# Performance work log

Hardware: AMD Instinct MI355X
Metric: run time of the kernel (lower is better)

Reference implementation:

```python
import jax, jax.numpy as jnp
import numpy as np
from jax import lax

B, N, D_IN = 256, 1024, 3
HID, ACT, HORIZON = 256, 6, 50


def _params(key):
    ks = jax.random.split(key, 24)
    w = lambda k, s: (jax.random.normal(k, s, jnp.float32) * 0.05)
    p = {}
    # PointNet encoder: per-point shared MLP 3->64->128->512, max-pool
    p['enc_w1'], p['enc_b1'] = w(ks[0], (D_IN, 64)), jnp.zeros((64,), jnp.float32)
    p['enc_w2'], p['enc_b2'] = w(ks[1], (64, 128)), jnp.zeros((128,), jnp.float32)
    p['enc_w3'], p['enc_b3'] = w(ks[2], (128, 512)), jnp.zeros((512,), jnp.float32)
    # mlp 512->256->128->hidden
    p['mlp_w1'], p['mlp_b1'] = w(ks[3], (512, 256)), jnp.zeros((256,), jnp.float32)
    p['mlp_w2'], p['mlp_b2'] = w(ks[4], (256, 128)), jnp.zeros((128,), jnp.float32)
    p['mlp_w3'], p['mlp_b3'] = w(ks[5], (128, HID)), jnp.zeros((HID,), jnp.float32)
    # GRU cell (PyTorch layout): W_ih [3H, in], W_hh [3H, H]
    p['W_ih'] = w(ks[6], (3 * HID, ACT))
    p['W_hh'] = w(ks[7], (3 * HID, HID))
    p['b_ih'] = jnp.zeros((3 * HID,), jnp.float32)
    p['b_hh'] = jnp.zeros((3 * HID,), jnp.float32)
    # out_mlp hidden->64->64->6
    p['out_w1'], p['out_b1'] = w(ks[8], (HID, 64)), jnp.zeros((64,), jnp.float32)
    p['out_w2'], p['out_b2'] = w(ks[9], (64, 64)), jnp.zeros((64,), jnp.float32)
    p['out_w3'], p['out_b3'] = w(ks[10], (64, ACT)), jnp.zeros((ACT,), jnp.float32)
    return p


def setup_inputs() -> dict:
    key = jax.random.key(0)
    k_data, k_p = jax.random.split(key)
    inp = {'data': jax.random.normal(k_data, (B, N, D_IN), jnp.float32), 'horizon': HORIZON}
    inp.update(_params(k_p))
    return inp


def reference(data, enc_w1, enc_b1, enc_w2, enc_b2, enc_w3, enc_b3,
              mlp_w1, mlp_b1, mlp_w2, mlp_b2, mlp_w3, mlp_b3,
              W_ih, W_hh, b_ih, b_hh,
              out_w1, out_b1, out_w2, out_b2, out_w3, out_b3,
              horizon):
    # PointNet encoder: shared per-point MLP + max-pool over points -> [B, 512]
    x = jax.nn.relu(data @ enc_w1 + enc_b1)
    x = jax.nn.relu(x @ enc_w2 + enc_b2)
    x = jax.nn.relu(x @ enc_w3 + enc_b3)
    h = jnp.max(x, axis=1)
    # init GRU hidden state
    g = jax.nn.relu(h @ mlp_w1 + mlp_b1)
    g = jax.nn.relu(g @ mlp_w2 + mlp_b2)
    gru_h = g @ mlp_w3 + mlp_b3  # [B, HID]

    def gru_cell(x_t, h_prev):
        gi = x_t @ W_ih.T + b_ih  # [B, 3H]
        gh = h_prev @ W_hh.T + b_hh
        i_r, i_z, i_n = jnp.split(gi, 3, axis=-1)
        h_r, h_z, h_n = jnp.split(gh, 3, axis=-1)
        r = jax.nn.sigmoid(i_r + h_r)
        z = jax.nn.sigmoid(i_z + h_z)
        n = jnp.tanh(i_n + r * h_n)
        return (1.0 - z) * n + z * h_prev

    def out_mlp(hh):
        o = jax.nn.relu(hh @ out_w1 + out_b1)
        o = jax.nn.relu(o @ out_w2 + out_b2)
        return o @ out_w3 + out_b3

    def step(carry, _):
        gi, gh_ = carry
        gh_ = gru_cell(gi, gh_)
        dw = out_mlp(gh_)
        gi = gi + dw
        return (gi, gh_), (dw, gi)

    init_in = jnp.zeros((data.shape[0], ACT), jnp.float32)
    _, (dws, ws) = lax.scan(step, (init_in, gru_h), None, length=int(horizon))
    # scan stacks time-first: [T, B, 6] -> [B, T, 6]
    return jnp.transpose(dws, (1, 0, 2)), jnp.transpose(ws, (1, 0, 2))
```

## Files before the change

### kernel.cpp

```cpp
#include <hip/hip_runtime.h>
#include <math.h>

#define B_    256
#define NPTS  1024
#define T_    50


__global__ __launch_bounds__(256) void prep_kernel(
    const float* __restrict__ whh, float* __restrict__ wp,
    unsigned* __restrict__ henc) {
  int idx = blockIdx.x * 256 + threadIdx.x;
  if (idx < 196608) {
    int c = idx & 3;
    int r = idx >> 2;
    int t2 = r & 255;
    int q = r >> 8;
    int j = q % 3;
    int k4 = q / 3;
    wp[idx] = whh[(j * 256 + t2) * 256 + (k4 * 4 + c)];
  }
  if (idx < 131072) henc[idx] = 0u;
}

__global__ __launch_bounds__(1024) void enc_kernel(
    const float* __restrict__ data,
    const float* __restrict__ w1, const float* __restrict__ b1,
    const float* __restrict__ w2, const float* __restrict__ b2,
    const float* __restrict__ w3, const float* __restrict__ b3,
    unsigned* __restrict__ henc) {
  __shared__ float h2t[2][128][66];
  const int t = threadIdx.x;
  const int b = blockIdx.x >> 1;
  const int half = blockIdx.x & 1;
  const int lane = t & 63;
  const int wv = __builtin_amdgcn_readfirstlane(t >> 6);

  float m[32];
#pragma unroll
  for (int o = 0; o < 32; ++o) m[o] = 0.0f;
  const float* __restrict__ w3b = w3 + wv * 32;

#pragma unroll 1
  for (int pair = 0; pair < 4; ++pair) {
#pragma unroll
    for (int tt = 0; tt < 2; ++tt) {
      const int ptg = b * NPTS + half * 512 + (pair * 2 + tt) * 64 + lane;
      const float x0 = data[ptg * 3], x1 = data[ptg * 3 + 1], x2 = data[ptg * 3 + 2];
      float a[8];
#pragma unroll
      for (int c = 0; c < 8; ++c) a[c] = b2[wv * 8 + c];
#pragma unroll 4
      for (int j = 0; j < 64; ++j) {
        float hj = fmaf(x0, w1[j], fmaf(x1, w1[64 + j], fmaf(x2, w1[128 + j], b1[j])));
        hj = fmaxf(hj, 0.0f);
        const float* __restrict__ w2r = w2 + j * 128 + wv * 8;
#pragma unroll
        for (int c = 0; c < 8; ++c) a[c] = fmaf(hj, w2r[c], a[c]);
      }
#pragma unroll
      for (int c = 0; c < 8; ++c) h2t[tt][wv * 8 + c][lane] = fmaxf(a[c], 0.0f);
    }
    __syncthreads();

    float acc0[32], acc1[32];
#pragma unroll
    for (int o = 0; o < 32; ++o) {
      acc0[o] = b3[wv * 32 + o];
      acc1[o] = acc0[o];
    }
#pragma unroll 4
    for (int k = 0; k < 128; ++k) {
      const float hk0 = h2t[0][k][lane];
      const float hk1 = h2t[1][k][lane];
      const float* __restrict__ wr = w3b + k * 512;
#pragma unroll
      for (int o = 0; o < 32; ++o) {
        const float w = wr[o];
        acc0[o] = fmaf(hk0, w, acc0[o]);
        acc1[o] = fmaf(hk1, w, acc1[o]);
      }
    }
#pragma unroll
    for (int o = 0; o < 32; ++o)
      m[o] = fmaxf(fmaxf(m[o], acc0[o]), acc1[o]);
    __syncthreads();
  }

#pragma unroll
  for (int off = 32; off > 0; off >>= 1) {
#pragma unroll
    for (int o = 0; o < 32; ++o) m[o] = fmaxf(m[o], __shfl_xor(m[o], off, 64));
  }
  if (lane == 0) {
    unsigned* __restrict__ hr = henc + b * 512 + wv * 32;
#pragma unroll
    for (int o = 0; o < 32; ++o) atomicMax(hr + o, __float_as_uint(m[o]));
  }
}

__device__ __forceinline__ double fexp(double x) {
  const double n = rint(x * 1.44269504088896338700e+00);
  const double r = fma(-n, 1.90821492927058770002e-10,
                       fma(-n, 6.93147180369123816490e-01, x));
  double p = 1.0 / 6227020800.0;
  p = fma(p, r, 1.0 / 479001600.0);
  p = fma(p, r, 1.0 / 39916800.0);
  p = fma(p, r, 1.0 / 3628800.0);
  p = fma(p, r, 1.0 / 362880.0);
  p = fma(p, r, 1.0 / 40320.0);
  p = fma(p, r, 1.0 / 5040.0);
  p = fma(p, r, 1.0 / 720.0);
  p = fma(p, r, 1.0 / 120.0);
  p = fma(p, r, 1.0 / 24.0);
  p = fma(p, r, 1.0 / 6.0);
  p = fma(p, r, 0.5);
  p = fma(p, r, 1.0);
  p = fma(p, r, 1.0);
  return ldexp(p, (int)n);
}
__device__ __forceinline__ double fsigm(double x) { return 1.0 / (1.0 + fexp(-x)); }
__device__ __forceinline__ double ftanh(double y) {
  const double e = fexp(-2.0 * y);
  return (1.0 - e) / (1.0 + e);
}

__global__ __launch_bounds__(576) void gru_kernel(
    const float* __restrict__ henc,
    const float* __restrict__ mw1, const float* __restrict__ mb1,
    const float* __restrict__ mw2, const float* __restrict__ mb2,
    const float* __restrict__ mw3, const float* __restrict__ mb3,
    const float* __restrict__ wih, const float* __restrict__ wp,
    const float* __restrict__ bih, const float* __restrict__ bhh,
    const float* __restrict__ ow1, const float* __restrict__ ob1,
    const float* __restrict__ ow2, const float* __restrict__ ob2,
    const float* __restrict__ ow3, const float* __restrict__ ob3,
    float* __restrict__ dout) {
  __shared__ __align__(16) double h_l[256];
  __shared__ double pp[3][256];
  __shared__ __align__(16) float ow1f[16384];
  __shared__ __align__(16) float ow2f[4096];
  __shared__ float ow3f[384];
  __shared__ float wihf[4608];
  __shared__ float bihf[768];
  __shared__ double o1_l[64];
  __shared__ double o2_l[64];
  __shared__ double gia_l[6];

  const int t = threadIdx.x;
  const int s = blockIdx.x;

  for (int i = t; i < 4608; i += 576) wihf[i] = wih[i];
  for (int i = t; i < 768; i += 576) bihf[i] = bih[i];

  double* const g1_l = (double*)ow1f;
  double* const g2_l = (double*)ow1f + 256;

  if (t < 256) {
    const float* __restrict__ hrow = henc + (s << 9);
    double a = (double)mb1[t];
#pragma unroll 4
    for (int k = 0; k < 512; ++k)
      a = fma((double)hrow[k], (double)mw1[k * 256 + t], a);
    g1_l[t] = fmax(a, 0.0);
  }
  __syncthreads();
  if (t < 128) {
    double a = (double)mb2[t];
#pragma unroll 4
    for (int k = 0; k < 256; ++k) a = fma(g1_l[k], (double)mw2[k * 128 + t], a);
    g2_l[t] = fmax(a, 0.0);
  }
  __syncthreads();
  if (t < 256) {
    double a = (double)mb3[t];
#pragma unroll 4
    for (int k = 0; k < 128; ++k) a = fma(g2_l[k], (double)mw3[k * 256 + t], a);
    h_l[t] = a;
  }
  if (t < 6) gia_l[t] = 0.0;
  __syncthreads();

  for (int i = t; i < 16384; i += 576) ow1f[i] = ow1[i];
  for (int i = t; i < 4096; i += 576) ow2f[i] = ow2[i];
  if (t < 384) ow3f[t] = ow3[t];

  const int c = t & 255;
  const int hh = (t >> 8) & 1;
  const int khome = hh << 5;
  const double br = (t < 512 && hh == 0) ? (double)bhh[c] : 0.0;
  const double bz = (t < 512 && hh == 0) ? (double)bhh[256 + c] : 0.0;
  const double bn = (t < 512 && hh == 0) ? (double)bhh[512 + c] : 0.0;
  double hreg = (t < 256) ? h_l[c] : 0.0;
  const float* const wpc = wp + c * 4;

  const int ln = t & 63;
  double ob1d = 0.0, ob2d = 0.0, ob3d = 0.0;
  if (t >= 512) {
    ob1d = (double)ob1[ln];
    ob2d = (double)ob2[ln];
    if (ln < 6) ob3d = (double)ob3[ln];
  }

  double ar, az, an;

#define MV_K(kk) {                                                           \
    const float* p_ = wpc + (khome + (kk)) * 3072;                           \
    const float4 wr = *(const float4*)(p_);                                  \
    const float4 wz = *(const float4*)(p_ + 1024);                           \
    const float4 wn = *(const float4*)(p_ + 2048);                           \
    const double2 ha = *(const double2*)(h_l + ((khome + (kk)) << 2));       \
    const double2 hb = *(const double2*)(h_l + ((khome + (kk)) << 2) + 2);   \
    ar = fma(ha.x, (double)wr.x, ar); ar = fma(ha.y, (double)wr.y, ar);      \
    ar = fma(hb.x, (double)wr.z, ar); ar = fma(hb.y, (double)wr.w, ar);      \
    az = fma(ha.x, (double)wz.x, az); az = fma(ha.y, (double)wz.y, az);      \
    az = fma(hb.x, (double)wz.z, az); az = fma(hb.y, (double)wz.w, az);      \
    an = fma(ha.x, (double)wn.x, an); an = fma(ha.y, (double)wn.y, an);      \
    an = fma(hb.x, (double)wn.z, an); an = fma(hb.y, (double)wn.w, an);      \
  }

  if (t < 512) {
    ar = br; az = bz; an = bn;
#pragma unroll 2
    for (int kk = 0; kk < 32; ++kk) MV_K(kk)
    if (hh) { pp[0][c] = ar; pp[1][c] = az; pp[2][c] = an; }
  }
  __syncthreads();

#pragma unroll 1
  for (int step = 0; step < T_; ++step) {
    if (t < 256) {
      const double cr = ar + pp[0][c];
      const double cz = az + pp[1][c];
      const double cn = an + pp[2][c];
      double gr = (double)bihf[c], gz = (double)bihf[256 + c],
             gn = (double)bihf[512 + c];
#pragma unroll
      for (int a = 0; a < 6; ++a) {
        const double xa = gia_l[a];
        gr = fma((double)wihf[c * 6 + a], xa, gr);
        gz = fma((double)wihf[(256 + c) * 6 + a], xa, gz);
        gn = fma((double)wihf[(512 + c) * 6 + a], xa, gn);
      }
      const double rv = fsigm(cr + gr);
      const double zv = fsigm(cz + gz);
      const double nv = ftanh(fma(rv, cn, gn));
      hreg = fma(zv, hreg - nv, nv);
      h_l[c] = hreg;
    }
    if (t < 512) { ar = br; az = bz; an = bn; }
    __syncthreads();

    if (t < 512) {
#pragma unroll 2
      for (int kk = 0; kk < 32; ++kk) MV_K(kk)
      if (hh) { pp[0][c] = ar; pp[1][c] = az; pp[2][c] = an; }
    } else {
      double a0 = ob1d, a1 = 0.0;
#pragma unroll 4
      for (int k = 0; k < 128; ++k) {
        a0 = fma(h_l[k], (double)ow1f[k * 64 + ln], a0);
        a1 = fma(h_l[128 + k], (double)ow1f[(128 + k) * 64 + ln], a1);
      }
      o1_l[ln] = fmax(a0 + a1, 0.0);
      __builtin_amdgcn_wave_barrier();
      double b0 = ob2d;
#pragma unroll 4
      for (int k = 0; k < 64; ++k)
        b0 = fma(o1_l[k], (double)ow2f[k * 64 + ln], b0);
      o2_l[ln] = fmax(b0, 0.0);
      __builtin_amdgcn_wave_barrier();
      if (ln < 6) {
        double a = ob3d;
#pragma unroll 4
        for (int k = 0; k < 64; ++k)
          a = fma(o2_l[k], (double)ow3f[k * 6 + ln], a);
        const double gi_new = gia_l[ln] + a;
        gia_l[ln] = gi_new;
        dout[s * 300 + step * 6 + ln] = (float)a;
        dout[76800 + s * 300 + step * 6 + ln] = (float)gi_new;
      }
    }
    __syncthreads();
  }
#undef MV_K
}

extern "C" void kernel_launch(void* const* d_in, const int* in_sizes, int n_in,
                              void* d_out, int out_size, void* d_ws, size_t ws_size,
                              hipStream_t stream) {
  const float* data = (const float*)d_in[0];
  const float* ew1 = (const float*)d_in[2];
  const float* eb1 = (const float*)d_in[3];
  const float* ew2 = (const float*)d_in[4];
  const float* eb2 = (const float*)d_in[5];
  const float* ew3 = (const float*)d_in[6];
  const float* eb3 = (const float*)d_in[7];
  const float* mw1 = (const float*)d_in[8];
  const float* mb1 = (const float*)d_in[9];
  const float* mw2 = (const float*)d_in[10];
  const float* mb2 = (const float*)d_in[11];
  const float* mw3 = (const float*)d_in[12];
  const float* mb3 = (const float*)d_in[13];
  const float* wih = (const float*)d_in[14];
  const float* whh = (const float*)d_in[15];
  const float* bih = (const float*)d_in[16];
  const float* bhh = (const float*)d_in[17];
  const float* ow1 = (const float*)d_in[18];
  const float* ob1 = (const float*)d_in[19];
  const float* ow2 = (const float*)d_in[20];
  const float* ob2 = (const float*)d_in[21];
  const float* ow3 = (const float*)d_in[22];
  const float* ob3 = (const float*)d_in[23];
  float* out = (float*)d_out;

  char* ws = (char*)d_ws;
  float*    wp   = (float*)(ws);
  unsigned* henc = (unsigned*)(ws + 786432);

  prep_kernel<<<768, 256, 0, stream>>>(whh, wp, henc);
  enc_kernel<<<512, 1024, 0, stream>>>(data, ew1, eb1, ew2, eb2, ew3, eb3, henc);
  gru_kernel<<<256, 576, 0, stream>>>((const float*)henc,
                                      mw1, mb1, mw2, mb2, mw3, mb3,
                                      wih, wp, bih, bhh,
                                      ow1, ob1, ow2, ob2, ow3, ob3,
                                      out);
}
```

Before: 1.132 ms.

## Stream GRU recurrent weights via async global-to-LDS ring buffer in matvec

Replaces the direct global float4 loads of the packed W_hh in the per-step GRU matvec with a 5-deep per-wave ring buffer in shared memory, filled by global_load_lds DMA with explicit waitcnt gating. This is meant to hide global memory latency behind the FMAs. To free LDS for the ring, the out_mlp weights ow1/ow2 are no longer staged in shared memory and are read from global each step instead. The hand-written waitcnt/sched_barrier sequencing is fragile, and the output-MLP wave now pays global latency.

```diff
diff --git a/kernel.cpp b/kernel.cpp
--- a/kernel.cpp
+++ b/kernel.cpp
@@ -124,6 +124,12 @@
   return (1.0 - e) / (1.0 + e);
 }
 
+typedef __attribute__((address_space(1))) unsigned int gls_gt;
+typedef __attribute__((address_space(3))) unsigned int gls_lt;
+__device__ __forceinline__ void dma16(const float* g, float* l) {
+  __builtin_amdgcn_global_load_lds((gls_gt*)g, (gls_lt*)l, 16, 0, 0);
+}
+
 __global__ __launch_bounds__(576) void gru_kernel(
     const float* __restrict__ henc,
     const float* __restrict__ mw1, const float* __restrict__ mb1,
@@ -135,13 +141,12 @@
     const float* __restrict__ ow2, const float* __restrict__ ob2,
     const float* __restrict__ ow3, const float* __restrict__ ob3,
     float* __restrict__ dout) {
+  __shared__ __align__(16) float stage_f[30720];
   __shared__ __align__(16) double h_l[256];
   __shared__ double pp[3][256];
-  __shared__ __align__(16) float ow1f[16384];
-  __shared__ __align__(16) float ow2f[4096];
-  __shared__ float ow3f[384];
   __shared__ float wihf[4608];
   __shared__ float bihf[768];
+  __shared__ float ow3f[384];
   __shared__ double o1_l[64];
   __shared__ double o2_l[64];
   __shared__ double gia_l[6];
@@ -151,9 +156,10 @@
 
   for (int i = t; i < 4608; i += 576) wihf[i] = wih[i];
   for (int i = t; i < 768; i += 576) bihf[i] = bih[i];
-
-  double* const g1_l = (double*)ow1f;
-  double* const g2_l = (double*)ow1f + 256;
+  if (t < 384) ow3f[t] = ow3[t];
+
+  double* const g1_l = (double*)stage_f;
+  double* const g2_l = (double*)stage_f + 256;
 
   if (t < 256) {
     const float* __restrict__ hrow = henc + (s << 9);
@@ -180,18 +186,17 @@
   if (t < 6) gia_l[t] = 0.0;
   __syncthreads();
 
-  for (int i = t; i < 16384; i += 576) ow1f[i] = ow1[i];
-  for (int i = t; i < 4096; i += 576) ow2f[i] = ow2[i];
-  if (t < 384) ow3f[t] = ow3[t];
-
   const int c = t & 255;
   const int hh = (t >> 8) & 1;
   const int khome = hh << 5;
+  const int w = t >> 6;
+  const int lane = t & 63;
+  const int cbase = (w & 3) << 6;
+  float* const swv = stage_f + w * 3840;
   const double br = (t < 512 && hh == 0) ? (double)bhh[c] : 0.0;
   const double bz = (t < 512 && hh == 0) ? (double)bhh[256 + c] : 0.0;
   const double bn = (t < 512 && hh == 0) ? (double)bhh[512 + c] : 0.0;
   double hreg = (t < 256) ? h_l[c] : 0.0;
-  const float* const wpc = wp + c * 4;
 
   const int ln = t & 63;
   double ob1d = 0.0, ob2d = 0.0, ob3d = 0.0;
@@ -202,26 +207,56 @@
   }
 
   double ar, az, an;
-
-#define MV_K(kk) {                                                           \
-    const float* p_ = wpc + (khome + (kk)) * 3072;                           \
-    const float4 wr = *(const float4*)(p_);                                  \
-    const float4 wz = *(const float4*)(p_ + 1024);                           \
-    const float4 wn = *(const float4*)(p_ + 2048);                           \
-    const double2 ha = *(const double2*)(h_l + ((khome + (kk)) << 2));       \
-    const double2 hb = *(const double2*)(h_l + ((khome + (kk)) << 2) + 2);   \
-    ar = fma(ha.x, (double)wr.x, ar); ar = fma(ha.y, (double)wr.y, ar);      \
-    ar = fma(hb.x, (double)wr.z, ar); ar = fma(hb.y, (double)wr.w, ar);      \
-    az = fma(ha.x, (double)wz.x, az); az = fma(ha.y, (double)wz.y, az);      \
-    az = fma(hb.x, (double)wz.z, az); az = fma(hb.y, (double)wz.w, az);      \
-    an = fma(ha.x, (double)wn.x, an); an = fma(ha.y, (double)wn.y, an);      \
-    an = fma(hb.x, (double)wn.z, an); an = fma(hb.y, (double)wn.w, an);      \
+  float4 wr4, wz4, wn4;
+  int acnt = 0, bcv = 0;
+
+#define CNS_LD(BUF) {                                                        \
+    asm volatile("s_waitcnt vmcnt(12)" ::: "memory");                        \
+    __builtin_amdgcn_sched_barrier(0);                                       \
+    const float* lb = swv + (BUF) * 768 + (lane << 2);                       \
+    wr4 = *(const float4*)(lb);                                              \
+    wz4 = *(const float4*)(lb + 256);                                        \
+    wn4 = *(const float4*)(lb + 512);                                        \
+  }
+
+#define STG(K4, BUF) {                                                       \
+    asm volatile("s_waitcnt lgkmcnt(0)" ::: "memory");                       \
+    __builtin_amdgcn_sched_barrier(0);                                       \
+    const float* gp = wp + (((K4) * 768 + cbase + lane) << 2);               \
+    float* lp = swv + (BUF) * 768;                                           \
+    dma16(gp, lp);                                                           \
+    dma16(gp + 1024, lp + 256);                                              \
+    dma16(gp + 2048, lp + 512);                                              \
+  }
+
+#define CNS_FMA(K4) {                                                        \
+    const double2 ha = *(const double2*)(h_l + ((K4) << 2));                 \
+    const double2 hb = *(const double2*)(h_l + ((K4) << 2) + 2);             \
+    ar = fma(ha.x, (double)wr4.x, ar); ar = fma(ha.y, (double)wr4.y, ar);    \
+    ar = fma(hb.x, (double)wr4.z, ar); ar = fma(hb.y, (double)wr4.w, ar);    \
+    az = fma(ha.x, (double)wz4.x, az); az = fma(ha.y, (double)wz4.y, az);    \
+    az = fma(hb.x, (double)wz4.z, az); az = fma(hb.y, (double)wz4.w, az);    \
+    an = fma(ha.x, (double)wn4.x, an); an = fma(ha.y, (double)wn4.y, an);    \
+    an = fma(hb.x, (double)wn4.z, an); an = fma(hb.y, (double)wn4.w, an);    \
+  }
+
+#define MV_PASS() {                                                          \
+    _Pragma("unroll 1")                                                      \
+    for (int ci = 0; ci < 32; ++ci) {                                        \
+      const int a_ = acnt + ci;                                              \
+      CNS_LD(bcv)                                                            \
+      STG(khome + ((a_ + 5) & 31), bcv)                                      \
+      CNS_FMA(khome + (a_ & 31))                                             \
+      bcv = (bcv == 4) ? 0 : bcv + 1;                                        \
+    }                                                                        \
+    acnt += 32;                                                              \
   }
 
   if (t < 512) {
+    STG(khome + 0, 0) STG(khome + 1, 1) STG(khome + 2, 2)
+    STG(khome + 3, 3) STG(khome + 4, 4)
     ar = br; az = bz; an = bn;
-#pragma unroll 2
-    for (int kk = 0; kk < 32; ++kk) MV_K(kk)
+    MV_PASS()
     if (hh) { pp[0][c] = ar; pp[1][c] = az; pp[2][c] = an; }
   }
   __syncthreads();
@@ -251,22 +286,21 @@
     __syncthreads();
 
     if (t < 512) {
-#pragma unroll 2
-      for (int kk = 0; kk < 32; ++kk) MV_K(kk)
+      MV_PASS()
       if (hh) { pp[0][c] = ar; pp[1][c] = az; pp[2][c] = an; }
     } else {
       double a0 = ob1d, a1 = 0.0;
 #pragma unroll 4
       for (int k = 0; k < 128; ++k) {
-        a0 = fma(h_l[k], (double)ow1f[k * 64 + ln], a0);
-        a1 = fma(h_l[128 + k], (double)ow1f[(128 + k) * 64 + ln], a1);
+        a0 = fma(h_l[k], (double)ow1[k * 64 + ln], a0);
+        a1 = fma(h_l[128 + k], (double)ow1[(128 + k) * 64 + ln], a1);
       }
       o1_l[ln] = fmax(a0 + a1, 0.0);
       __builtin_amdgcn_wave_barrier();
       double b0 = ob2d;
 #pragma unroll 4
       for (int k = 0; k < 64; ++k)
-        b0 = fma(o1_l[k], (double)ow2f[k * 64 + ln], b0);
+        b0 = fma(o1_l[k], (double)ow2[k * 64 + ln], b0);
       o2_l[ln] = fmax(b0, 0.0);
       __builtin_amdgcn_wave_barrier();
       if (ln < 6) {
@@ -282,7 +316,10 @@
     }
     __syncthreads();
   }
-#undef MV_K
+#undef CNS_LD
+#undef STG
+#undef CNS_FMA
+#undef MV_PASS
 }
 
 extern "C" void kernel_launch(void* const* d_in, const int* in_sizes, int n_in,
```

Result: slower. 1.275 ms (+12.7%).
